# Kernel optimization log

Measured on AMD Instinct MI355X. Metric: run time of the kernel, lower is better.

The kernel has to match this reference:

```python
import math
import jax, jax.numpy as jnp
import numpy as np

B, DIM, C, N = 1024, 512, 1000, 8
R = 0.05
WEIGHT_LAMBDA = 0.3
CN = C * N
TOPK = math.ceil(R * CN)  # 400


def setup_inputs() -> dict:
    key = jax.random.key(0)
    k1, k2, k3 = jax.random.split(key, 3)
    x = jax.random.normal(k1, (B, DIM), dtype=jnp.float32)
    # kaiming_uniform_(a=sqrt(5)) on a (DIM, CN) tensor: fan_in = CN (torch 2D fan_in = size(1)),
    # gain = sqrt(2/(1+a^2)) = sqrt(1/3), bound = gain * sqrt(3/fan_in)
    bound = math.sqrt(1.0 / 3.0) * math.sqrt(3.0 / CN)
    proxies = jax.random.uniform(k2, (DIM, CN), dtype=jnp.float32, minval=-bound, maxval=bound)
    target = jax.random.randint(k3, (B,), 0, C)
    return {"x": x, "proxies": proxies, "target": target}


def reference(x, proxies, target):
    instance_label = jnp.repeat(jnp.arange(C), N)  # (CN,)

    # F.normalize(Proxies, p=2, dim=0) with eps=1e-12 clamp
    norm = jnp.maximum(jnp.linalg.norm(proxies, axis=0, keepdims=True), 1e-12)
    centers = proxies / norm  # (DIM, CN)

    similarity = x @ centers  # (B, CN)

    positive_mask = (target[:, None] == instance_label[None, :]).astype(similarity.dtype)

    # topk over similarity boosted so all positives are included, then scatter 1s
    _, idx = jax.lax.top_k(similarity + 1000.0 * positive_mask, TOPK)  # (B, TOPK)
    mask = jnp.zeros_like(similarity).at[jnp.arange(B)[:, None], idx].set(1.0)
    mask = jax.lax.stop_gradient(mask)

    prob_a = mask * similarity  # (B, CN)
    # matmul with block one-hot y_instance_onehot == sum over the N proxies of each class
    logits = prob_a.reshape(B, C, N).sum(axis=-1)  # (B, C)

    logits_mask = jax.lax.stop_gradient((logits != 0.0).astype(logits.dtype))
    exp_l = jnp.exp(logits) * logits_mask
    predict = exp_l / (1e-8 + exp_l.sum(axis=1, keepdims=True))

    # sum(-y_onehot * log(predict+1e-20), 1) == -log(predict[b, target[b]] + 1e-20)
    loss_classify = jnp.mean(-jnp.log(predict[jnp.arange(B), target] + 1e-20))

    # regularizer: (centers.T @ centers) @ y_instance_onehot, fused as
    # centers.T @ (per-class sum of centers) -- identical math, avoids the CNxCN matrix
    centers_cls = centers.reshape(DIM, C, N).sum(axis=-1)  # (DIM, C)
    centers_logits = centers.T @ centers_cls  # (CN, C)
    logp = jax.nn.log_softmax(centers_logits, axis=1)
    reg = -jnp.mean(logp[jnp.arange(CN), instance_label])

    total = loss_classify + WEIGHT_LAMBDA * reg
    return (total, loss_classify)
```

## Files before the change

### kernel.cpp

```cpp
#include <hip/hip_runtime.h>
#include <hip/hip_bf16.h>
#include <math.h>

#define PB   1024
#define PDIM 512
#define PC   1000
#define PN   8
#define PCN  8000
#define PTOPK 400
#define NONPOS_K 392
#define NBIN 1024
#define CANDMAX 1024

typedef __bf16 bf16x8 __attribute__((ext_vector_type(8)));
typedef __bf16 bf16x4 __attribute__((ext_vector_type(4)));
typedef float  f32x4  __attribute__((ext_vector_type(4)));

__device__ static inline void async_load16(const __bf16* g, __bf16* l) {
    __builtin_amdgcn_global_load_lds(
        (const __attribute__((address_space(1))) void*)g,
        (__attribute__((address_space(3))) void*)l,
        16, 0, 0);
}

__device__ static inline unsigned bf16bits(float v) {
    __bf16 b = (__bf16)v;
    unsigned short u;
    __builtin_memcpy(&u, &b, 2);
    return (unsigned)u;
}

__global__ __launch_bounds__(256) void k_prep(const float* __restrict__ x,
                                              const float* __restrict__ P,
                                              __bf16* __restrict__ xb,
                                              __bf16* __restrict__ Pt,
                                              __bf16* __restrict__ ccls,
                                              float* __restrict__ esd,
                                              float* __restrict__ padf,
                                              float* __restrict__ acc) {
    int bid = blockIdx.x, tid = threadIdx.x;
    if (bid < 125) {
        __shared__ float t[64][65];
        __shared__ float red[4][64];
        __shared__ float sinv[64];
        int j0 = bid * 64;
        int tx = tid & 63, ty = tid >> 6;
        {
            const float* pc = P + (size_t)(ty * 128) * PCN + j0 + tx;
            float ss = 0.f;
#pragma unroll 8
            for (int k = 0; k < 128; ++k) {
                float v = pc[(size_t)k * PCN];
                ss = fmaf(v, v, ss);
            }
            red[ty][tx] = ss;
        }
        __syncthreads();
        if (tid < 64) {
            float sq = red[0][tid] + red[1][tid] + red[2][tid] + red[3][tid];
            sinv[tid] = 1.0f / fmaxf(sqrtf(sq), 1e-12f);
        }
        for (int dc = 0; dc < 8; ++dc) {
            __syncthreads();
#pragma unroll
            for (int rr = 0; rr < 16; ++rr) {
                int d = dc * 64 + ty * 16 + rr;
                t[ty * 16 + rr][tx] = P[(size_t)d * PCN + j0 + tx];
            }
            __syncthreads();
            float cs0 = 0.f, cs1 = 0.f;
#pragma unroll
            for (int rr = 0; rr < 16; ++rr) {
                int jj = ty * 16 + rr;
                float val = t[tx][jj] * sinv[jj];
                Pt[(size_t)(j0 + jj) * PDIM + dc * 64 + tx] = (__bf16)val;
                if (rr < 8) cs0 += val; else cs1 += val;
            }
            int c0 = (j0 >> 3) + ty * 2;
            ccls[(size_t)c0 * PDIM + dc * 64 + tx] = (__bf16)cs0;
            ccls[(size_t)(c0 + 1) * PDIM + dc * 64 + tx] = (__bf16)cs1;
        }
    } else if (bid < 637) {
        int i = (bid - 125) * 256 + tid;
        float4 v = ((const float4*)x)[i];
        bf16x4 o;
        o[0] = (__bf16)v.x; o[1] = (__bf16)v.y; o[2] = (__bf16)v.z; o[3] = (__bf16)v.w;
        ((bf16x4*)xb)[i] = o;
    } else {
        if (bid == 637 && tid < 16) acc[tid] = 0.f;
        int i = (bid - 637) * 256 + tid;
        if (i < 16000) esd[i] = 0.f;
        else if (i < 16000 + 6144) padf[i - 16000] = 0.f;
    }
}

__global__ __launch_bounds__(512, 2) void k_gemms2(const __bf16* __restrict__ xb,
                                                   const __bf16* __restrict__ Pt,
                                                   const __bf16* __restrict__ ccls,
                                                   __bf16* __restrict__ simb,
                                                   float* __restrict__ esum,
                                                   float* __restrict__ diag) {
    __shared__ __align__(16) __bf16 As[2][256 * 64];
    __shared__ __align__(16) __bf16 Bs[2][256 * 64];

    int tid = threadIdx.x;
    int w = tid >> 6, lane = tid & 63;
    int wr = w >> 2, wc = w & 3;
    int quad = lane >> 4, l15 = lane & 15;

    int bid = blockIdx.x;
    bool is_sim = bid < 128;
    int M0, N0, Amax, Bmax;
    const __bf16 *Ab, *Bb;
    if (is_sim) {
        int mt = bid >> 5, nt = bid & 31;
        M0 = mt * 256; N0 = nt * 256;
        Ab = xb; Bb = Pt; Amax = PB - 1; Bmax = PCN - 1;
    } else {
        int b2 = bid - 128;
        int mt = b2 >> 2, nt = b2 & 3;
        M0 = mt * 256; N0 = nt * 256;
        Ab = Pt; Bb = ccls; Amax = PCN - 1; Bmax = 1023;
    }

    f32x4 acc[8][4] = {};

#define STAGE(kt_) {                                                         \
    int k0_ = (kt_) * 64, bb_ = (kt_) & 1;                                   \
    _Pragma("unroll")                                                        \
    for (int p_ = 0; p_ < 4; ++p_) {                                         \
        int idx_ = p_ * 512 + tid;                                           \
        int row_ = idx_ >> 3, sp_ = idx_ & 7;                                \
        int gk_ = ((sp_ ^ (row_ & 7)) << 3) + k0_;                           \
        int ga_ = M0 + row_; if (ga_ > Amax) ga_ = Amax;                     \
        async_load16(Ab + (size_t)ga_ * PDIM + gk_, &As[bb_][idx_ * 8]);     \
        int gb_ = N0 + row_; if (gb_ > Bmax) gb_ = Bmax;                     \
        async_load16(Bb + (size_t)gb_ * PDIM + gk_, &Bs[bb_][idx_ * 8]);     \
    } }

    STAGE(0)
    for (int kt = 0; kt < 8; ++kt) {
        int cur = kt & 1;
        asm volatile("s_waitcnt lgkmcnt(0)" ::: "memory");
        __builtin_amdgcn_s_barrier();
        if (kt < 7) {
            STAGE(kt + 1)
            asm volatile("s_waitcnt vmcnt(8)" ::: "memory");
        } else {
            asm volatile("s_waitcnt vmcnt(0)" ::: "memory");
        }
        __builtin_amdgcn_s_barrier();

#pragma unroll
        for (int ks = 0; ks < 2; ++ks) {
            bf16x8 af[8], bfr[4];
#pragma unroll
            for (int mi = 0; mi < 8; ++mi) {
                int row = wr * 128 + mi * 16 + l15;
                af[mi] = *(const bf16x8*)&As[cur][(row << 6) +
                         ((((ks << 2) + quad) ^ (row & 7)) << 3)];
            }
#pragma unroll
            for (int nj = 0; nj < 4; ++nj) {
                int row = wc * 64 + nj * 16 + l15;
                bfr[nj] = *(const bf16x8*)&Bs[cur][(row << 6) +
                          ((((ks << 2) + quad) ^ (row & 7)) << 3)];
            }
            __builtin_amdgcn_s_setprio(1);
#pragma unroll
            for (int mi = 0; mi < 8; ++mi)
#pragma unroll
                for (int nj = 0; nj < 4; ++nj)
                    acc[mi][nj] = __builtin_amdgcn_mfma_f32_16x16x32_bf16(
                        af[mi], bfr[nj], acc[mi][nj], 0, 0, 0);
            __builtin_amdgcn_s_setprio(0);
        }
    }
#undef STAGE

    if (is_sim) {
#pragma unroll
        for (int mi = 0; mi < 8; ++mi) {
            int r0 = M0 + wr * 128 + mi * 16 + quad * 4;
#pragma unroll
            for (int nj = 0; nj < 4; ++nj) {
                int cc = N0 + wc * 64 + nj * 16 + l15;
#pragma unroll
                for (int r = 0; r < 4; ++r) {
                    unsigned p = bf16bits(acc[mi][nj][r]);
                    unsigned q = (unsigned)__shfl_xor((int)p, 1, 64);
                    if (((l15 & 1) == 0) && cc < PCN)
                        *(unsigned*)&simb[(size_t)(r0 + r) * PCN + cc] = p | (q << 16);
                }
            }
        }
    } else {
#pragma unroll
        for (int mi = 0; mi < 8; ++mi) {
            int r0 = M0 + wr * 128 + mi * 16 + quad * 4;
            float psum[4] = {0.f, 0.f, 0.f, 0.f};
#pragma unroll
            for (int nj = 0; nj < 4; ++nj) {
                int cc = N0 + wc * 64 + nj * 16 + l15;
                bool cvalid = (cc < PC);
#pragma unroll
                for (int r = 0; r < 4; ++r) {
                    float v = acc[mi][nj][r];
                    psum[r] += cvalid ? expf(v) : 0.f;
                    int rr = r0 + r;
                    if (cvalid && rr < PCN && cc == (rr >> 3)) diag[rr] = v;
                }
            }
#pragma unroll
            for (int off = 1; off < 16; off <<= 1)
#pragma unroll
                for (int r = 0; r < 4; ++r)
                    psum[r] += __shfl_xor(psum[r], off, 64);
            if (l15 == 0) {
#pragma unroll
                for (int r = 0; r < 4; ++r) {
                    int rr = r0 + r;
                    if (rr < PCN) atomicAdd(&esum[rr], psum[r]);
                }
            }
        }
    }
}

__global__ __launch_bounds__(256) void k_rowloss(const __bf16* __restrict__ sim,
                                                 const int* __restrict__ target,
                                                 float* __restrict__ acc) {
    __shared__ unsigned hist[NBIN];
    __shared__ float redf[8];
    __shared__ unsigned wtot[4];
    __shared__ float cand[CANDMAX];
    __shared__ unsigned candn;
    __shared__ int s_bin, s_A;
    __shared__ float s_tau;
    __shared__ int s_gt, s_eq;
    __shared__ float s_et;

    int b = blockIdx.x, tid = threadIdx.x;
    int lane = tid & 63, wv = tid >> 6;
    const bf16x8* row8 = (const bf16x8*)(sim + (size_t)b * PCN);
    int targ = target[b];

#pragma unroll
    for (int k = 0; k < 4; ++k) hist[tid + 256 * k] = 0u;
    if (tid == 0) candn = 0u;

    float pv[4][8];
    float lmn = INFINITY, lmx = -INFINITY;
#pragma unroll
    for (int k = 0; k < 4; ++k) {
        int c = tid + 256 * k;
        if (c < PC) {
            bf16x8 vv = row8[c];
#pragma unroll
            for (int n = 0; n < 8; ++n) pv[k][n] = (float)vv[n];
            if (c != targ) {
#pragma unroll
                for (int n = 0; n < 8; ++n) {
                    lmn = fminf(lmn, pv[k][n]);
                    lmx = fmaxf(lmx, pv[k][n]);
                }
            }
        } else {
#pragma unroll
            for (int n = 0; n < 8; ++n) pv[k][n] = 0.f;
        }
    }
    for (int off = 32; off; off >>= 1) {
        lmn = fminf(lmn, __shfl_down(lmn, off, 64));
        lmx = fmaxf(lmx, __shfl_down(lmx, off, 64));
    }
    if (lane == 0) { redf[wv] = lmn; redf[4 + wv] = lmx; }
    __syncthreads();
    float lo = fminf(fminf(redf[0], redf[1]), fminf(redf[2], redf[3]));
    float hi = fmaxf(fmaxf(redf[4], redf[5]), fmaxf(redf[6], redf[7]));
    float range = hi - lo;
    float scale = (range > 0.f) ? (float)NBIN / range : 0.f;

#pragma unroll
    for (int k = 0; k < 4; ++k) {
        int c = tid + 256 * k;
        if (c < PC && c != targ) {
#pragma unroll
            for (int n = 0; n < 8; ++n) {
                int bin = (int)((pv[k][n] - lo) * scale);
                bin = bin < 0 ? 0 : (bin > NBIN - 1 ? NBIN - 1 : bin);
                atomicAdd(&hist[bin], 1u);
            }
        }
    }
    __syncthreads();

    int b0 = tid * 4;
    unsigned h0 = hist[b0], h1 = hist[b0 + 1], h2 = hist[b0 + 2], h3 = hist[b0 + 3];
    unsigned l3 = h3, l2 = h2 + l3, l1 = h1 + l2, l0 = h0 + l1;
    unsigned T = l0;
#pragma unroll
    for (int step = 1; step < 64; step <<= 1) {
        unsigned u = __shfl_down(T, step, 64);
        if (lane + step < 64) T += u;
    }
    if (lane == 0) wtot[wv] = T;
    __syncthreads();
    unsigned tail = 0;
#pragma unroll
    for (int w2 = 0; w2 < 4; ++w2) if (w2 > wv) tail += wtot[w2];
    unsigned E = T - l0 + tail;
    {
        unsigned sfx[4] = {l0 + E, l1 + E, l2 + E, l3 + E};
        unsigned nxt[4] = {l1 + E, l2 + E, l3 + E, E};
#pragma unroll
        for (int i = 0; i < 4; ++i)
            if (sfx[i] >= NONPOS_K && nxt[i] < NONPOS_K) {
                s_bin = b0 + i;
                s_A = (int)nxt[i];
            }
    }
    __syncthreads();
    int tbin = s_bin, A = s_A;

#pragma unroll
    for (int k = 0; k < 4; ++k) {
        int c = tid + 256 * k;
        if (c < PC && c != targ) {
#pragma unroll
            for (int n = 0; n < 8; ++n) {
                int bin = (int)((pv[k][n] - lo) * scale);
                bin = bin < 0 ? 0 : (bin > NBIN - 1 ? NBIN - 1 : bin);
                if (bin == tbin) {
                    unsigned idx = atomicAdd(&candn, 1u);
                    if (idx < CANDMAX) cand[idx] = pv[k][n];
                }
            }
        }
    }
    __syncthreads();
    int m = (int)candn; if (m > CANDMAX) m = CANDMAX;
    int rank = NONPOS_K - A;
    for (int ci = tid; ci < m; ci += 256) {
        float val = cand[ci];
        int g = 0, e = 0;
        for (int i = 0; i < m; ++i) {
            g += cand[i] > val;
            e += cand[i] == val;
        }
        if (g < rank && rank <= g + e) { s_tau = val; s_gt = g; s_eq = e; }
    }
    __syncthreads();
    float tau = s_tau;
    int cgt = A + s_gt, ceq = s_eq;
    int rem = NONPOS_K - cgt;
    bool all_eq = (rem >= ceq);

    int offs[4] = {0, 0, 0, 0};
    if (!all_eq) {
        unsigned chunk_base = 0;
#pragma unroll
        for (int k = 0; k < 4; ++k) {
            int c = tid + 256 * k;
            unsigned tn = 0;
            if (c < PC && c != targ) {
#pragma unroll
                for (int n = 0; n < 8; ++n) tn += (pv[k][n] == tau) ? 1u : 0u;
            }
            unsigned inc = tn;
#pragma unroll
            for (int step = 1; step < 64; step <<= 1) {
                unsigned u = __shfl_up(inc, step, 64);
                if (lane >= step) inc += u;
            }
            __syncthreads();
            if (lane == 63) wtot[wv] = inc;
            __syncthreads();
            unsigned base = 0;
#pragma unroll
            for (int w2 = 0; w2 < 4; ++w2) if (w2 < wv) base += wtot[w2];
            offs[k] = (int)(chunk_base + base + inc - tn);
            chunk_base += wtot[0] + wtot[1] + wtot[2] + wtot[3];
        }
    }

    float psum = 0.f;
#pragma unroll
    for (int k = 0; k < 4; ++k) {
        int c = tid + 256 * k;
        if (c >= PC) continue;
        float lg = 0.f;
        if (c == targ) {
#pragma unroll
            for (int n = 0; n < 8; ++n) lg += pv[k][n];
        } else {
#pragma unroll
            for (int n = 0; n < 8; ++n) {
                float v = pv[k][n];
                bool sel = v > tau;
                if (!sel && v == tau) {
                    if (all_eq) sel = true;
                    else { sel = (offs[k] < rem); offs[k]++; }
                }
                if (sel) lg += v;
            }
        }
        float e = (lg != 0.0f) ? expf(lg) : 0.0f;
        psum += e;
        if (c == targ) s_et = e;
    }
    for (int off = 32; off; off >>= 1) psum += __shfl_down(psum, off, 64);
    if (lane == 0) redf[wv] = psum;
    __syncthreads();
    if (tid == 0) {
        float denom = 1e-8f + redf[0] + redf[1] + redf[2] + redf[3];
        atomicAdd(acc, -logf(s_et / denom + 1e-20f));
    }
}

__global__ __launch_bounds__(256) void k_final(const float* __restrict__ esum,
                                               const float* __restrict__ diag,
                                               const float* __restrict__ acc,
                                               float* __restrict__ out) {
    __shared__ float redf[4];
    int tid = threadIdx.x, lane = tid & 63, wv = tid >> 6;
    float s = 0.f;
    for (int j = tid; j < PCN; j += 256)
        s += logf(esum[j]) - diag[j];
    for (int off = 32; off; off >>= 1) s += __shfl_down(s, off, 64);
    if (lane == 0) redf[wv] = s;
    __syncthreads();
    if (tid == 0) {
        float rg = (redf[0] + redf[1] + redf[2] + redf[3]) * (1.0f / PCN);
        float lc = acc[0] * (1.0f / PB);
        out[0] = lc + 0.3f * rg;
        out[1] = lc;
    }
}

extern "C" void kernel_launch(void* const* d_in, const int* in_sizes, int n_in,
                              void* d_out, int out_size, void* d_ws, size_t ws_size,
                              hipStream_t stream) {
    const float* x       = (const float*)d_in[0];
    const float* proxies = (const float*)d_in[1];
    const int*   target  = (const int*)d_in[2];
    float* out = (float*)d_out;
    float* ws  = (float*)d_ws;

    float*  acc   = ws;
    float*  esum  = ws + 64064;
    float*  diag  = ws + 72064;
    __bf16* xb    = (__bf16*)(ws + 80064);
    __bf16* cclsb = (__bf16*)(ws + 342208);
    __bf16* Pt    = (__bf16*)(ws + 604352);
    __bf16* simb  = (__bf16*)(ws + 2652352);

    float* padf = (float*)cclsb + 256000;

    k_prep<<<725, 256, 0, stream>>>(x, proxies, xb, Pt, cclsb, esum, padf, acc);
    k_gemms2<<<256, 512, 0, stream>>>(xb, Pt, cclsb, simb, esum, diag);
    k_rowloss<<<PB, 256, 0, stream>>>(simb, target, acc);
    k_final<<<1, 256, 0, stream>>>(esum, diag, acc, out);
}
```

Before: 140.7 us.

## Replace min/max histogram and candidate sort with two-level radix select on bf16 keys

The per-row top-k threshold search no longer reduces min/max and bins floats into a range histogram followed by an O(m^2) candidate ranking. It maps each bf16 value to an order-preserving 16-bit key and does a two-pass radix select: 1024 bins on the high 10 bits, then 64 bins on the low 6 bits inside the chosen bin. This drops a block reduction, the candidate buffer and the quadratic compare loop, and the threshold becomes exact with no CANDMAX overflow risk. Tie handling now compares keys, which is exact because values are bf16.

```diff
diff --git a/kernel.cpp b/kernel.cpp
--- a/kernel.cpp
+++ b/kernel.cpp
@@ -10,7 +10,6 @@
 #define PTOPK 400
 #define NONPOS_K 392
 #define NBIN 1024
-#define CANDMAX 1024
 
 typedef __bf16 bf16x8 __attribute__((ext_vector_type(8)));
 typedef __bf16 bf16x4 __attribute__((ext_vector_type(4)));
@@ -231,13 +230,10 @@
                                                  const int* __restrict__ target,
                                                  float* __restrict__ acc) {
     __shared__ unsigned hist[NBIN];
+    __shared__ unsigned hist2[64];
     __shared__ float redf[8];
     __shared__ unsigned wtot[4];
-    __shared__ float cand[CANDMAX];
-    __shared__ unsigned candn;
-    __shared__ int s_bin, s_A;
-    __shared__ float s_tau;
-    __shared__ int s_gt, s_eq;
+    __shared__ unsigned s_cb, s_A, s_tauk, s_gt, s_eq;
     __shared__ float s_et;
 
     int b = blockIdx.x, tid = threadIdx.x;
@@ -247,50 +243,38 @@
 
 #pragma unroll
     for (int k = 0; k < 4; ++k) hist[tid + 256 * k] = 0u;
-    if (tid == 0) candn = 0u;
+    if (tid < 64) hist2[tid] = 0u;
 
     float pv[4][8];
-    float lmn = INFINITY, lmx = -INFINITY;
+    unsigned kv[4][8];
 #pragma unroll
     for (int k = 0; k < 4; ++k) {
         int c = tid + 256 * k;
         if (c < PC) {
             bf16x8 vv = row8[c];
 #pragma unroll
-            for (int n = 0; n < 8; ++n) pv[k][n] = (float)vv[n];
-            if (c != targ) {
-#pragma unroll
-                for (int n = 0; n < 8; ++n) {
-                    lmn = fminf(lmn, pv[k][n]);
-                    lmx = fmaxf(lmx, pv[k][n]);
-                }
+            for (int n = 0; n < 8; ++n) {
+                __bf16 e = vv[n];
+                pv[k][n] = (float)e;
+                unsigned short u;
+                __builtin_memcpy(&u, &e, 2);
+                kv[k][n] = (u & 0x8000u) ? (unsigned)(unsigned short)~u
+                                         : (unsigned)(u | 0x8000u);
             }
         } else {
 #pragma unroll
-            for (int n = 0; n < 8; ++n) pv[k][n] = 0.f;
-        }
-    }
-    for (int off = 32; off; off >>= 1) {
-        lmn = fminf(lmn, __shfl_down(lmn, off, 64));
-        lmx = fmaxf(lmx, __shfl_down(lmx, off, 64));
-    }
-    if (lane == 0) { redf[wv] = lmn; redf[4 + wv] = lmx; }
-    __syncthreads();
-    float lo = fminf(fminf(redf[0], redf[1]), fminf(redf[2], redf[3]));
-    float hi = fmaxf(fmaxf(redf[4], redf[5]), fmaxf(redf[6], redf[7]));
-    float range = hi - lo;
-    float scale = (range > 0.f) ? (float)NBIN / range : 0.f;
+            for (int n = 0; n < 8; ++n) { pv[k][n] = 0.f; kv[k][n] = 0u; }
+        }
+    }
+    __syncthreads();
 
 #pragma unroll
     for (int k = 0; k < 4; ++k) {
         int c = tid + 256 * k;
         if (c < PC && c != targ) {
 #pragma unroll
-            for (int n = 0; n < 8; ++n) {
-                int bin = (int)((pv[k][n] - lo) * scale);
-                bin = bin < 0 ? 0 : (bin > NBIN - 1 ? NBIN - 1 : bin);
-                atomicAdd(&hist[bin], 1u);
-            }
+            for (int n = 0; n < 8; ++n)
+                atomicAdd(&hist[kv[k][n] >> 6], 1u);
         }
     }
     __syncthreads();
@@ -316,45 +300,44 @@
 #pragma unroll
         for (int i = 0; i < 4; ++i)
             if (sfx[i] >= NONPOS_K && nxt[i] < NONPOS_K) {
-                s_bin = b0 + i;
-                s_A = (int)nxt[i];
-            }
-    }
-    __syncthreads();
-    int tbin = s_bin, A = s_A;
+                s_cb = (unsigned)(b0 + i);
+                s_A = nxt[i];
+            }
+    }
+    __syncthreads();
+    unsigned cb = s_cb, A = s_A;
 
 #pragma unroll
     for (int k = 0; k < 4; ++k) {
         int c = tid + 256 * k;
         if (c < PC && c != targ) {
 #pragma unroll
-            for (int n = 0; n < 8; ++n) {
-                int bin = (int)((pv[k][n] - lo) * scale);
-                bin = bin < 0 ? 0 : (bin > NBIN - 1 ? NBIN - 1 : bin);
-                if (bin == tbin) {
-                    unsigned idx = atomicAdd(&candn, 1u);
-                    if (idx < CANDMAX) cand[idx] = pv[k][n];
-                }
-            }
-        }
-    }
-    __syncthreads();
-    int m = (int)candn; if (m > CANDMAX) m = CANDMAX;
-    int rank = NONPOS_K - A;
-    for (int ci = tid; ci < m; ci += 256) {
-        float val = cand[ci];
-        int g = 0, e = 0;
-        for (int i = 0; i < m; ++i) {
-            g += cand[i] > val;
-            e += cand[i] == val;
-        }
-        if (g < rank && rank <= g + e) { s_tau = val; s_gt = g; s_eq = e; }
-    }
-    __syncthreads();
-    float tau = s_tau;
-    int cgt = A + s_gt, ceq = s_eq;
-    int rem = NONPOS_K - cgt;
-    bool all_eq = (rem >= ceq);
+            for (int n = 0; n < 8; ++n)
+                if ((kv[k][n] >> 6) == cb)
+                    atomicAdd(&hist2[kv[k][n] & 63u], 1u);
+        }
+    }
+    __syncthreads();
+
+    if (wv == 0) {
+        unsigned h = hist2[lane];
+        unsigned sfx = h;
+#pragma unroll
+        for (int step = 1; step < 64; step <<= 1) {
+            unsigned u = __shfl_down(sfx, step, 64);
+            if (lane + step < 64) sfx += u;
+        }
+        unsigned nxt = sfx - h;
+        if (A + sfx >= NONPOS_K && A + nxt < NONPOS_K) {
+            s_tauk = (cb << 6) | (unsigned)lane;
+            s_gt = A + nxt;
+            s_eq = h;
+        }
+    }
+    __syncthreads();
+    unsigned tauk = s_tauk;
+    int rem = NONPOS_K - (int)s_gt;
+    bool all_eq = (rem >= (int)s_eq);
 
     int offs[4] = {0, 0, 0, 0};
     if (!all_eq) {
@@ -365,7 +348,7 @@
             unsigned tn = 0;
             if (c < PC && c != targ) {
 #pragma unroll
-                for (int n = 0; n < 8; ++n) tn += (pv[k][n] == tau) ? 1u : 0u;
+                for (int n = 0; n < 8; ++n) tn += (kv[k][n] == tauk) ? 1u : 0u;
             }
             unsigned inc = tn;
 #pragma unroll
@@ -396,13 +379,12 @@
         } else {
 #pragma unroll
             for (int n = 0; n < 8; ++n) {
-                float v = pv[k][n];
-                bool sel = v > tau;
-                if (!sel && v == tau) {
+                bool sel = kv[k][n] > tauk;
+                if (!sel && kv[k][n] == tauk) {
                     if (all_eq) sel = true;
                     else { sel = (offs[k] < rem); offs[k]++; }
                 }
-                if (sel) lg += v;
+                if (sel) lg += pv[k][n];
             }
         }
         float e = (lg != 0.0f) ? expf(lg) : 0.0f;
```

Measured after the change: 144.2 us. +2.5%, slower.

## Interleave prefetch, LDS fragment loads and MFMA in quarter steps of GEMM loop

Applied to the files above, without the earlier changes.

Restructures the double-buffered GEMM main loop so that the next tile's global-to-LDS loads are issued in halves between quarter-sized MFMA groups, and A fragments are read from LDS just before each group. It removes the barrier that separated staging from compute and uses sched_barrier to keep the interleaving. The aim is to hide global and LDS latency behind MFMA work, at the cost of a single vmcnt(0) wait per iteration and tighter reliance on scheduling order.

```diff
diff --git a/kernel.cpp b/kernel.cpp
--- a/kernel.cpp
+++ b/kernel.cpp
@@ -125,58 +125,83 @@
 
     f32x4 acc[8][4] = {};
 
-#define STAGE(kt_) {                                                         \
-    int k0_ = (kt_) * 64, bb_ = (kt_) & 1;                                   \
-    _Pragma("unroll")                                                        \
-    for (int p_ = 0; p_ < 4; ++p_) {                                         \
-        int idx_ = p_ * 512 + tid;                                           \
+#define STAGE_HALF_A(buf_, h_, k0_) {                                        \
+    _Pragma("unroll")                                                        \
+    for (int p_ = 0; p_ < 2; ++p_) {                                         \
+        int idx_ = (h_) * 1024 + p_ * 512 + tid;                             \
         int row_ = idx_ >> 3, sp_ = idx_ & 7;                                \
-        int gk_ = ((sp_ ^ (row_ & 7)) << 3) + k0_;                           \
-        int ga_ = M0 + row_; if (ga_ > Amax) ga_ = Amax;                     \
-        async_load16(Ab + (size_t)ga_ * PDIM + gk_, &As[bb_][idx_ * 8]);     \
-        int gb_ = N0 + row_; if (gb_ > Bmax) gb_ = Bmax;                     \
-        async_load16(Bb + (size_t)gb_ * PDIM + gk_, &Bs[bb_][idx_ * 8]);     \
+        int gk_ = ((sp_ ^ (row_ & 7)) << 3) + (k0_);                         \
+        int g_ = M0 + row_; if (g_ > Amax) g_ = Amax;                        \
+        async_load16(Ab + (size_t)g_ * PDIM + gk_, &As[buf_][idx_ * 8]);     \
     } }
-
-    STAGE(0)
+#define STAGE_HALF_B(buf_, h_, k0_) {                                        \
+    _Pragma("unroll")                                                        \
+    for (int p_ = 0; p_ < 2; ++p_) {                                         \
+        int idx_ = (h_) * 1024 + p_ * 512 + tid;                             \
+        int row_ = idx_ >> 3, sp_ = idx_ & 7;                                \
+        int gk_ = ((sp_ ^ (row_ & 7)) << 3) + (k0_);                         \
+        int g_ = N0 + row_; if (g_ > Bmax) g_ = Bmax;                        \
+        async_load16(Bb + (size_t)g_ * PDIM + gk_, &Bs[buf_][idx_ * 8]);     \
+    } }
+
+#define AF_LOAD(m2_, mi_) {                                                  \
+    int row_ = wr * 128 + (mi_) * 16 + l15;                                  \
+    _Pragma("unroll")                                                        \
+    for (int ks_ = 0; ks_ < 2; ++ks_)                                        \
+        af[m2_][ks_] = *(const bf16x8*)&As[cur][(row_ << 6) +                \
+                       ((((ks_ << 2) + quad) ^ (row_ & 7)) << 3)];           \
+    }
+
+#define MFMA16(q_)                                                           \
+    __builtin_amdgcn_s_setprio(1);                                           \
+    _Pragma("unroll")                                                        \
+    for (int m2_ = 0; m2_ < 2; ++m2_)                                        \
+    _Pragma("unroll")                                                        \
+    for (int nj_ = 0; nj_ < 4; ++nj_)                                        \
+    _Pragma("unroll")                                                        \
+    for (int ks_ = 0; ks_ < 2; ++ks_)                                        \
+        acc[(q_) * 2 + m2_][nj_] = __builtin_amdgcn_mfma_f32_16x16x32_bf16(  \
+            af[m2_][ks_], bfr[nj_][ks_], acc[(q_) * 2 + m2_][nj_], 0, 0, 0); \
+    __builtin_amdgcn_s_setprio(0);                                           \
+    __builtin_amdgcn_sched_barrier(0);
+
+    STAGE_HALF_A(0, 0, 0) STAGE_HALF_A(0, 1, 0)
+    STAGE_HALF_B(0, 0, 0) STAGE_HALF_B(0, 1, 0)
+    asm volatile("s_waitcnt vmcnt(0)" ::: "memory");
+    __builtin_amdgcn_s_barrier();
+
     for (int kt = 0; kt < 8; ++kt) {
-        int cur = kt & 1;
-        asm volatile("s_waitcnt lgkmcnt(0)" ::: "memory");
+        int cur = kt & 1, nxt = cur ^ 1;
+        int k1 = (kt + 1) << 6;
+        bool pf = (kt < 7);
+
+        bf16x8 bfr[4][2], af[2][2];
+#pragma unroll
+        for (int nj = 0; nj < 4; ++nj) {
+            int row = wc * 64 + nj * 16 + l15;
+#pragma unroll
+            for (int ks = 0; ks < 2; ++ks)
+                bfr[nj][ks] = *(const bf16x8*)&Bs[cur][(row << 6) +
+                              ((((ks << 2) + quad) ^ (row & 7)) << 3)];
+        }
+        AF_LOAD(0, 0) AF_LOAD(1, 1)
+        if (pf) { STAGE_HALF_A(nxt, 0, k1) STAGE_HALF_B(nxt, 0, k1) }
+        MFMA16(0)
+        AF_LOAD(0, 2) AF_LOAD(1, 3)
+        if (pf) { STAGE_HALF_A(nxt, 1, k1) STAGE_HALF_B(nxt, 1, k1) }
+        MFMA16(1)
+        AF_LOAD(0, 4) AF_LOAD(1, 5)
+        MFMA16(2)
+        AF_LOAD(0, 6) AF_LOAD(1, 7)
+        MFMA16(3)
+
+        asm volatile("s_waitcnt vmcnt(0)" ::: "memory");
         __builtin_amdgcn_s_barrier();
-        if (kt < 7) {
-            STAGE(kt + 1)
-            asm volatile("s_waitcnt vmcnt(8)" ::: "memory");
-        } else {
-            asm volatile("s_waitcnt vmcnt(0)" ::: "memory");
-        }
-        __builtin_amdgcn_s_barrier();
-
-#pragma unroll
-        for (int ks = 0; ks < 2; ++ks) {
-            bf16x8 af[8], bfr[4];
-#pragma unroll
-            for (int mi = 0; mi < 8; ++mi) {
-                int row = wr * 128 + mi * 16 + l15;
-                af[mi] = *(const bf16x8*)&As[cur][(row << 6) +
-                         ((((ks << 2) + quad) ^ (row & 7)) << 3)];
-            }
-#pragma unroll
-            for (int nj = 0; nj < 4; ++nj) {
-                int row = wc * 64 + nj * 16 + l15;
-                bfr[nj] = *(const bf16x8*)&Bs[cur][(row << 6) +
-                          ((((ks << 2) + quad) ^ (row & 7)) << 3)];
-            }
-            __builtin_amdgcn_s_setprio(1);
-#pragma unroll
-            for (int mi = 0; mi < 8; ++mi)
-#pragma unroll
-                for (int nj = 0; nj < 4; ++nj)
-                    acc[mi][nj] = __builtin_amdgcn_mfma_f32_16x16x32_bf16(
-                        af[mi], bfr[nj], acc[mi][nj], 0, 0, 0);
-            __builtin_amdgcn_s_setprio(0);
-        }
-    }
-#undef STAGE
+    }
+#undef STAGE_HALF_A
+#undef STAGE_HALF_B
+#undef AF_LOAD
+#undef MFMA16
 
     if (is_sim) {
 #pragma unroll
```

Measured after the change: 141.1 us. Within noise of the previous version (+0.3%).
